# Performance work log

Measured on AMD Instinct MI355X. Metric: run time of the kernel, lower is better.

The kernel has to match this reference:

```python
import jax, jax.numpy as jnp
import numpy as np


def setup_inputs() -> dict:
    key = jax.random.key(0)
    k1, k2 = jax.random.split(key)
    B, M, N, D = 8, 2048, 2048, 1024
    x = jax.random.normal(k1, (B, M, D), dtype=jnp.float32)
    y = jax.random.normal(k2, (B, N, D), dtype=jnp.float32)
    return {"x": x, "y": y}


def reference(x, y):
    # scores e[b,m,n] = <x[b,m], y[b,n]>   (K.batch_dot(x, y, axes=2))
    e = jnp.einsum('bmd,bnd->bmn', x, y)
    # stable softmax over last axis (the exp/max/sum sequence in the original)
    p = jax.nn.softmax(e, axis=-1)
    # K.batch_dot(z, x, axes=1): contract axis 1 (m) of both -> [B, n, d]; V = x
    out = jnp.einsum('bmn,bmd->bnd', p, x)
    return out
```

## Files before the change

kernel.cpp:

```cpp
#include <hip/hip_runtime.h>
#include <hip/hip_bf16.h>
#include <stdint.h>

#define B_ 8
#define M_ 2048
#define N_ 2048
#define D_ 1024

typedef __bf16 bf16x8 __attribute__((ext_vector_type(8)));
typedef float f32x4 __attribute__((ext_vector_type(4)));
typedef uint16_t us4 __attribute__((ext_vector_type(4)));
typedef uint16_t us8 __attribute__((ext_vector_type(8)));

__device__ __forceinline__ uint16_t f2b(float f) {
    uint32_t u = __float_as_uint(f);
    return (uint16_t)((u + 0x7FFFu + ((u >> 16) & 1u)) >> 16);
}
__device__ __forceinline__ float b2f(uint16_t h) {
    return __uint_as_float(((uint32_t)h) << 16);
}

__device__ __forceinline__ void gld16(const uint16_t* g, const uint16_t* l) {
    __builtin_amdgcn_global_load_lds(
        (const __attribute__((address_space(1))) uint32_t*)g,
        (__attribute__((address_space(3))) uint32_t*)l,
        16, 0, 0);
}

__global__ __launch_bounds__(256) void k_split(const float* __restrict__ x,
                                               const float* __restrict__ y,
                                               uint16_t* __restrict__ xh, uint16_t* __restrict__ xl,
                                               uint16_t* __restrict__ yh, uint16_t* __restrict__ yl) {
    const int i = (blockIdx.x * 256 + threadIdx.x) * 4;
    float4 vx = *(const float4*)(x + i);
    float4 vy = *(const float4*)(y + i);
    float fx[4] = {vx.x, vx.y, vx.z, vx.w};
    float fy[4] = {vy.x, vy.y, vy.z, vy.w};
    us4 hx, lx, hy, ly;
#pragma unroll
    for (int k = 0; k < 4; ++k) {
        uint16_t h = f2b(fx[k]);
        hx[k] = h; lx[k] = f2b(fx[k] - b2f(h));
        uint16_t g = f2b(fy[k]);
        hy[k] = g; ly[k] = f2b(fy[k] - b2f(g));
    }
    *(us4*)(xh + i) = hx;
    *(us4*)(xl + i) = lx;
    *(us4*)(yh + i) = hy;
    *(us4*)(yl + i) = ly;
}

__global__ __launch_bounds__(512, 4) void k_gemm1(const uint16_t* __restrict__ xh,
                                                  const uint16_t* __restrict__ xl,
                                                  const uint16_t* __restrict__ yh,
                                                  const uint16_t* __restrict__ yl,
                                                  float* __restrict__ e,
                                                  float* __restrict__ pmax,
                                                  float* __restrict__ psum) {
    const int b = blockIdx.z;
    const int m0 = blockIdx.x * 128;
    const int n0 = blockIdx.y * 128;
    __shared__ __align__(16) uint16_t lds[32768];

    const int tid = threadIdx.x;
    const int lane = tid & 63;
    const int wid = tid >> 6;
    const int wm = (wid >> 2) * 64;
    const int wn = (wid & 3) * 32;
    const int quad = lane >> 4;
    const int r16 = lane & 15;
    const int swz8 = (quad ^ ((r16 >> 1) & 3)) * 8;

    const int row0 = wid * 16 + (lane >> 2);
    const int gd8 = ((lane & 3) ^ ((row0 >> 1) & 3)) * 8;
    const uint16_t* sp[4];
    sp[0] = xh + ((size_t)b * M_ + m0 + row0) * D_ + gd8;
    sp[1] = xl + ((size_t)b * M_ + m0 + row0) * D_ + gd8;
    sp[2] = yh + ((size_t)b * N_ + n0 + row0) * D_ + gd8;
    sp[3] = yl + ((size_t)b * N_ + n0 + row0) * D_ + gd8;
    const int ldsW = wid * 512;

    auto STAGE = [&](int dst, int ktn) {
#pragma unroll
        for (int c = 0; c < 4; ++c)
            gld16(sp[c] + ktn * 32, &lds[dst + c * 4096 + ldsW]);
    };

    const int abase = (wm + r16) * 32 + swz8;
    const int bbase = 8192 + (wn + r16) * 32 + swz8;

    f32x4 acc[4][2];
#pragma unroll
    for (int i = 0; i < 4; ++i)
#pragma unroll
        for (int j = 0; j < 2; ++j) acc[i][j] = (f32x4){0.f, 0.f, 0.f, 0.f};

    STAGE(0, 0);
    __syncthreads();

    for (int kt = 0; kt < D_ / 32; ++kt) {
        const int bo = (kt & 1) << 14;
        const int nbo = bo ^ 16384;
        if (kt < D_ / 32 - 1) STAGE(nbo, kt + 1);

        bf16x8 ah[4], al[4], bh[2], bl[2];
#pragma unroll
        for (int j = 0; j < 2; ++j) {
            bh[j] = *(const bf16x8*)&lds[bo + bbase + j * 512];
            bl[j] = *(const bf16x8*)&lds[bo + bbase + 4096 + j * 512];
        }
#pragma unroll
        for (int i = 0; i < 4; ++i) {
            ah[i] = *(const bf16x8*)&lds[bo + abase + i * 512];
            al[i] = *(const bf16x8*)&lds[bo + abase + 4096 + i * 512];
        }
#pragma unroll
        for (int i = 0; i < 4; ++i)
#pragma unroll
            for (int j = 0; j < 2; ++j) {
                acc[i][j] = __builtin_amdgcn_mfma_f32_16x16x32_bf16(ah[i], bh[j], acc[i][j], 0, 0, 0);
                acc[i][j] = __builtin_amdgcn_mfma_f32_16x16x32_bf16(ah[i], bl[j], acc[i][j], 0, 0, 0);
                acc[i][j] = __builtin_amdgcn_mfma_f32_16x16x32_bf16(al[i], bh[j], acc[i][j], 0, 0, 0);
            }
        __syncthreads();
    }

    float* eb = e + (size_t)b * M_ * N_;
    const int grows = (int)gridDim.z * M_;
    const int growbase = b * M_ + m0 + wm;
    const int nb = (n0 + wn) >> 5;
    float* pm = pmax + (size_t)nb * grows + growbase;
    float* ps = psum + (size_t)nb * grows + growbase;

#pragma unroll
    for (int i = 0; i < 4; ++i) {
#pragma unroll
        for (int r = 0; r < 4; ++r) {
            const float v0 = acc[i][0][r], v1 = acc[i][1][r];
            float mrow = fmaxf(v0, v1);
#pragma unroll
            for (int s = 1; s < 16; s <<= 1) mrow = fmaxf(mrow, __shfl_xor(mrow, s, 64));
            float srow_ = __expf(v0 - mrow) + __expf(v1 - mrow);
#pragma unroll
            for (int s = 1; s < 16; s <<= 1) srow_ += __shfl_xor(srow_, s, 64);
            const int lrow = i * 16 + quad * 4 + r;
            if (r16 == 0) { pm[lrow] = mrow; ps[lrow] = srow_; }
            const size_t ebase = (size_t)(m0 + wm + lrow) * N_ + n0 + wn + r16;
#pragma unroll
            for (int j = 0; j < 2; ++j) eb[ebase + j * 16] = acc[i][j][r];
        }
    }
}

__global__ __launch_bounds__(256) void k_combine(const float* __restrict__ pmax,
                                                 const float* __restrict__ psum,
                                                 float* __restrict__ mx,
                                                 float* __restrict__ inv, int rows) {
    const int r = blockIdx.x * 256 + threadIdx.x;
    float m = -3.4e38f;
#pragma unroll
    for (int nb = 0; nb < 64; ++nb) m = fmaxf(m, pmax[(size_t)nb * rows + r]);
    float s = 0.f;
#pragma unroll
    for (int nb = 0; nb < 64; ++nb)
        s += psum[(size_t)nb * rows + r] * __expf(pmax[(size_t)nb * rows + r] - m);
    mx[r] = m;
    inv[r] = 1.0f / s;
}

__global__ __launch_bounds__(256) void k_texp(const float* __restrict__ e,
                                              const float* __restrict__ mx,
                                              const float* __restrict__ inv,
                                              uint16_t* __restrict__ pT) {
    const int b = blockIdx.z, m0 = blockIdx.x * 64, n0 = blockIdx.y * 64;
    __shared__ float tile[64 * 65];
    const int t = threadIdx.x;
    const float* eb = e + (size_t)b * M_ * N_;
#pragma unroll
    for (int q = 0; q < 4; ++q) {
        const int row = q * 16 + (t >> 4);
        const int c4 = (t & 15) * 4;
        float4 v = *(const float4*)&eb[(size_t)(m0 + row) * N_ + n0 + c4];
        const float mv = mx[b * M_ + m0 + row];
        const float iv = inv[b * M_ + m0 + row];
        tile[row * 65 + c4 + 0] = __expf(v.x - mv) * iv;
        tile[row * 65 + c4 + 1] = __expf(v.y - mv) * iv;
        tile[row * 65 + c4 + 2] = __expf(v.z - mv) * iv;
        tile[row * 65 + c4 + 3] = __expf(v.w - mv) * iv;
    }
    __syncthreads();
    uint16_t* pb = pT + (size_t)b * N_ * M_;
#pragma unroll
    for (int q = 0; q < 2; ++q) {
        const int n = q * 32 + (t >> 3);
        const int mc = (t & 7) * 8;
        us8 o;
#pragma unroll
        for (int k = 0; k < 8; ++k) o[k] = f2b(tile[(mc + k) * 65 + n]);
        *(us8*)&pb[(size_t)(n0 + n) * M_ + m0 + mc] = o;
    }
}

__global__ __launch_bounds__(256) void k_tx(const float* __restrict__ x,
                                            uint16_t* __restrict__ xt) {
    const int b = blockIdx.z, m0 = blockIdx.x * 64, d0 = blockIdx.y * 64;
    __shared__ float tile[64 * 65];
    const int t = threadIdx.x;
    const float* xb = x + (size_t)b * M_ * D_;
#pragma unroll
    for (int q = 0; q < 4; ++q) {
        const int row = q * 16 + (t >> 4);
        const int c4 = (t & 15) * 4;
        float4 v = *(const float4*)&xb[(size_t)(m0 + row) * D_ + d0 + c4];
        tile[row * 65 + c4 + 0] = v.x;
        tile[row * 65 + c4 + 1] = v.y;
        tile[row * 65 + c4 + 2] = v.z;
        tile[row * 65 + c4 + 3] = v.w;
    }
    __syncthreads();
    uint16_t* xtb = xt + (size_t)b * D_ * M_;
#pragma unroll
    for (int q = 0; q < 2; ++q) {
        const int d = q * 32 + (t >> 3);
        const int mc = (t & 7) * 8;
        us8 o;
#pragma unroll
        for (int k = 0; k < 8; ++k) o[k] = f2b(tile[(mc + k) * 65 + d]);
        *(us8*)&xtb[(size_t)(d0 + d) * M_ + m0 + mc] = o;
    }
}

__global__ __launch_bounds__(256) void k_gemm2(const uint16_t* __restrict__ pT,
                                               const uint16_t* __restrict__ xt,
                                               float* __restrict__ out) {
    const int b = blockIdx.z;
    const int n0 = blockIdx.x * 128;
    const int d0 = blockIdx.y * 128;
    __shared__ __align__(16) uint16_t lds[32768];

    const int tid = threadIdx.x;
    const int lane = tid & 63;
    const int wid = tid >> 6;
    const int wn = (wid & 1) * 64;
    const int wd = (wid >> 1) * 64;
    const int quad = lane >> 4;
    const int r16 = lane & 15;

    const uint16_t* srcA = pT + ((size_t)b * N_ + n0) * M_;
    const uint16_t* srcB = xt + ((size_t)b * D_ + d0) * M_;

    f32x4 acc[4][4];
#pragma unroll
    for (int i = 0; i < 4; ++i)
#pragma unroll
        for (int j = 0; j < 4; ++j) acc[i][j] = (f32x4){0.f, 0.f, 0.f, 0.f};

    auto STAGE = [&](int dst, int kt) {
#pragma unroll
        for (int c = 0; c < 8; ++c) {
            const int offbase = c * 2048 + wid * 512;
            const int tile = offbase >> 13;
            const int o = (offbase & 8191) + lane * 8;
            const int row = o >> 6;
            const int gp = (o & 63) >> 3;
            const int gd = gp ^ (row & 7);
            const uint16_t* sp = tile ? srcB : srcA;
            gld16(sp + (size_t)row * M_ + kt * 64 + gd * 8, &lds[dst + offbase]);
        }
    };

    STAGE(0, 0);
    __syncthreads();

    for (int kt = 0; kt < M_ / 64; ++kt) {
        const int bo = (kt & 1) << 14;
        const int nbo = bo ^ 16384;
        if (kt < M_ / 64 - 1) STAGE(nbo, kt + 1);

#pragma unroll
        for (int h = 0; h < 2; ++h) {
            const int p = (h * 4 + quad) ^ (r16 & 7);
            bf16x8 a[4], bbr[4];
#pragma unroll
            for (int i = 0; i < 4; ++i) {
                a[i]   = *(const bf16x8*)&lds[bo + (wn + i * 16 + r16) * 64 + p * 8];
                bbr[i] = *(const bf16x8*)&lds[bo + 8192 + (wd + i * 16 + r16) * 64 + p * 8];
            }
#pragma unroll
            for (int i = 0; i < 4; ++i)
#pragma unroll
                for (int j = 0; j < 4; ++j)
                    acc[i][j] = __builtin_amdgcn_mfma_f32_16x16x32_bf16(a[i], bbr[j], acc[i][j], 0, 0, 0);
        }
        __syncthreads();
    }

    float* ob = out + (size_t)b * N_ * D_;
#pragma unroll
    for (int i = 0; i < 4; ++i) {
        const int rbase = n0 + wn + i * 16 + quad * 4;
#pragma unroll
        for (int j = 0; j < 4; ++j) {
            const int col = d0 + wd + j * 16 + r16;
#pragma unroll
            for (int r = 0; r < 4; ++r)
                ob[(size_t)(rbase + r) * D_ + col] = acc[i][j][r];
        }
    }
}

extern "C" void kernel_launch(void* const* d_in, const int* in_sizes, int n_in,
                              void* d_out, int out_size, void* d_ws, size_t ws_size,
                              hipStream_t stream) {
    const float* x = (const float*)d_in[0];
    const float* y = (const float*)d_in[1];
    float* out = (float*)d_out;
    char* ws = (char*)d_ws;

    const size_t MiB = 1024 * 1024;
    int g = 8;
    while (g > 1 && (size_t)g * 32 * MiB > ws_size) g >>= 1;
    if ((size_t)g * 32 * MiB > ws_size) return;

    const size_t T = (size_t)g * M_ * D_ * 2;
    uint16_t* xh = (uint16_t*)(ws + 0 * T);
    uint16_t* xl = (uint16_t*)(ws + 1 * T);
    uint16_t* yh = (uint16_t*)(ws + 2 * T);
    uint16_t* yl = (uint16_t*)(ws + 3 * T);
    float*    e  = (float*)(ws + 4 * T);
    float*    mx = (float*)(ws);
    float*    inv = mx + (size_t)g * M_;
    uint16_t* xt = xl;
    uint16_t* pT = yh;

    const size_t pelems = (size_t)64 * g * M_;
    float* pmax = (float*)d_out + (size_t)B_ * N_ * D_ - 2 * pelems;
    float* psum = pmax + pelems;

    for (int c0 = 0; c0 < B_; c0 += g) {
        const float* xc = x + (size_t)c0 * M_ * D_;
        const float* yc = y + (size_t)c0 * N_ * D_;
        float* oc = out + (size_t)c0 * N_ * D_;

        hipLaunchKernelGGL(k_split, dim3((g * M_ * D_) / (256 * 4)), dim3(256), 0, stream,
                           xc, yc, xh, xl, yh, yl);
        hipLaunchKernelGGL(k_gemm1, dim3(M_ / 128, N_ / 128, g), dim3(512), 0, stream,
                           xh, xl, yh, yl, e, pmax, psum);
        hipLaunchKernelGGL(k_combine, dim3((g * M_) / 256), dim3(256), 0, stream,
                           pmax, psum, mx, inv, g * M_);
        hipLaunchKernelGGL(k_texp, dim3(M_ / 64, N_ / 64, g), dim3(256), 0, stream,
                           e, mx, inv, pT);
        hipLaunchKernelGGL(k_tx, dim3(M_ / 64, D_ / 64, g), dim3(256), 0, stream, xc, xt);
        hipLaunchKernelGGL(k_gemm2, dim3(N_ / 128, D_ / 128, g), dim3(256), 0, stream,
                           pT, xt, oc);
    }
}
```

Measured before the change: 520.5 us.

## Enlarge gemm1 tile to 256x256 using 32x32x16 MFMA with s_setprio

The score GEMM's block tile grows from 128x128 to 256x256, and each wave now computes a 128x64 sub-tile with 32x32x16 bf16 MFMA instead of 16x16x32. LDS doubles to 128KB double-buffered, and each stage loads two 128-row halves per operand. The aim is more operand reuse per LDS read and fewer global loads per FLOP in the three-pass split-bf16 GEMM. The cost is lower occupancy (launch bound 2, fewer blocks: 256 instead of 1024), so there are fewer waves to hide latency and worse tail balance. The partial softmax max/sum blocks drop from 64 to 32 per row, and the combine kernel and workspace sizing change to match.

```diff
diff --git a/kernel.cpp b/kernel.cpp
--- a/kernel.cpp
+++ b/kernel.cpp
@@ -9,6 +9,7 @@
 
 typedef __bf16 bf16x8 __attribute__((ext_vector_type(8)));
 typedef float f32x4 __attribute__((ext_vector_type(4)));
+typedef float f32x16 __attribute__((ext_vector_type(16)));
 typedef uint16_t us4 __attribute__((ext_vector_type(4)));
 typedef uint16_t us8 __attribute__((ext_vector_type(8)));
 
@@ -50,7 +51,7 @@
     *(us4*)(yl + i) = ly;
 }
 
-__global__ __launch_bounds__(512, 4) void k_gemm1(const uint16_t* __restrict__ xh,
+__global__ __launch_bounds__(512, 2) void k_gemm1(const uint16_t* __restrict__ xh,
                                                   const uint16_t* __restrict__ xl,
                                                   const uint16_t* __restrict__ yh,
                                                   const uint16_t* __restrict__ yl,
@@ -58,96 +59,106 @@
                                                   float* __restrict__ pmax,
                                                   float* __restrict__ psum) {
     const int b = blockIdx.z;
-    const int m0 = blockIdx.x * 128;
-    const int n0 = blockIdx.y * 128;
-    __shared__ __align__(16) uint16_t lds[32768];
+    const int m0 = blockIdx.x * 256;
+    const int n0 = blockIdx.y * 256;
+    __shared__ __align__(16) uint16_t lds[65536];
 
     const int tid = threadIdx.x;
     const int lane = tid & 63;
     const int wid = tid >> 6;
-    const int wm = (wid >> 2) * 64;
-    const int wn = (wid & 3) * 32;
-    const int quad = lane >> 4;
-    const int r16 = lane & 15;
-    const int swz8 = (quad ^ ((r16 >> 1) & 3)) * 8;
-
-    const int row0 = wid * 16 + (lane >> 2);
-    const int gd8 = ((lane & 3) ^ ((row0 >> 1) & 3)) * 8;
-    const uint16_t* sp[4];
-    sp[0] = xh + ((size_t)b * M_ + m0 + row0) * D_ + gd8;
-    sp[1] = xl + ((size_t)b * M_ + m0 + row0) * D_ + gd8;
-    sp[2] = yh + ((size_t)b * N_ + n0 + row0) * D_ + gd8;
-    sp[3] = yl + ((size_t)b * N_ + n0 + row0) * D_ + gd8;
+    const int wm = (wid >> 2) * 128;
+    const int wn = (wid & 3) * 64;
+    const int l31 = lane & 31;
+    const int hi = lane >> 5;
+    const int swl = (l31 >> 1) & 3;
+
+    const int base_row = wid * 16 + (lane >> 2);
+    const int gd8 = ((lane & 3) ^ ((lane >> 3) & 3)) * 8;
+    const uint16_t* gp[4];
+    gp[0] = xh + ((size_t)b * M_ + m0 + base_row) * D_ + gd8;
+    gp[1] = xl + ((size_t)b * M_ + m0 + base_row) * D_ + gd8;
+    gp[2] = yh + ((size_t)b * N_ + n0 + base_row) * D_ + gd8;
+    gp[3] = yl + ((size_t)b * N_ + n0 + base_row) * D_ + gd8;
     const int ldsW = wid * 512;
 
     auto STAGE = [&](int dst, int ktn) {
 #pragma unroll
-        for (int c = 0; c < 4; ++c)
-            gld16(sp[c] + ktn * 32, &lds[dst + c * 4096 + ldsW]);
+        for (int c = 0; c < 8; ++c)
+            gld16(gp[c >> 1] + (size_t)(c & 1) * (128 * D_) + ktn * 32,
+                  &lds[dst + c * 4096 + ldsW]);
     };
 
-    const int abase = (wm + r16) * 32 + swz8;
-    const int bbase = 8192 + (wn + r16) * 32 + swz8;
-
-    f32x4 acc[4][2];
+    const int abase = (wm + l31) * 32;
+    const int bbase = 16384 + (wn + l31) * 32;
+
+    f32x16 acc[4][2];
 #pragma unroll
     for (int i = 0; i < 4; ++i)
 #pragma unroll
-        for (int j = 0; j < 2; ++j) acc[i][j] = (f32x4){0.f, 0.f, 0.f, 0.f};
+        for (int j = 0; j < 2; ++j)
+#pragma unroll
+            for (int r = 0; r < 16; ++r) acc[i][j][r] = 0.f;
 
     STAGE(0, 0);
     __syncthreads();
 
     for (int kt = 0; kt < D_ / 32; ++kt) {
-        const int bo = (kt & 1) << 14;
-        const int nbo = bo ^ 16384;
-        if (kt < D_ / 32 - 1) STAGE(nbo, kt + 1);
-
-        bf16x8 ah[4], al[4], bh[2], bl[2];
-#pragma unroll
-        for (int j = 0; j < 2; ++j) {
-            bh[j] = *(const bf16x8*)&lds[bo + bbase + j * 512];
-            bl[j] = *(const bf16x8*)&lds[bo + bbase + 4096 + j * 512];
-        }
-#pragma unroll
-        for (int i = 0; i < 4; ++i) {
-            ah[i] = *(const bf16x8*)&lds[bo + abase + i * 512];
-            al[i] = *(const bf16x8*)&lds[bo + abase + 4096 + i * 512];
-        }
-#pragma unroll
-        for (int i = 0; i < 4; ++i)
+        const int bo = (kt & 1) << 15;
+        if (kt < D_ / 32 - 1) STAGE(bo ^ 32768, kt + 1);
+
+#pragma unroll
+        for (int kc = 0; kc < 2; ++kc) {
+            const int g8 = ((hi + 2 * kc) ^ swl) * 8;
+            bf16x8 ah[4], al[4], bh[2], bl[2];
 #pragma unroll
             for (int j = 0; j < 2; ++j) {
-                acc[i][j] = __builtin_amdgcn_mfma_f32_16x16x32_bf16(ah[i], bh[j], acc[i][j], 0, 0, 0);
-                acc[i][j] = __builtin_amdgcn_mfma_f32_16x16x32_bf16(ah[i], bl[j], acc[i][j], 0, 0, 0);
-                acc[i][j] = __builtin_amdgcn_mfma_f32_16x16x32_bf16(al[i], bh[j], acc[i][j], 0, 0, 0);
+                const int o = bo + bbase + j * 1024 + g8;
+                bh[j] = *(const bf16x8*)&lds[o];
+                bl[j] = *(const bf16x8*)&lds[o + 8192];
             }
+#pragma unroll
+            for (int i = 0; i < 4; ++i) {
+                const int o = bo + abase + i * 1024 + g8;
+                ah[i] = *(const bf16x8*)&lds[o];
+                al[i] = *(const bf16x8*)&lds[o + 8192];
+            }
+            __builtin_amdgcn_s_setprio(1);
+#pragma unroll
+            for (int i = 0; i < 4; ++i)
+#pragma unroll
+                for (int j = 0; j < 2; ++j) {
+                    acc[i][j] = __builtin_amdgcn_mfma_f32_32x32x16_bf16(ah[i], bh[j], acc[i][j], 0, 0, 0);
+                    acc[i][j] = __builtin_amdgcn_mfma_f32_32x32x16_bf16(ah[i], bl[j], acc[i][j], 0, 0, 0);
+                    acc[i][j] = __builtin_amdgcn_mfma_f32_32x32x16_bf16(al[i], bh[j], acc[i][j], 0, 0, 0);
+                }
+            __builtin_amdgcn_s_setprio(0);
+        }
         __syncthreads();
     }
 
     float* eb = e + (size_t)b * M_ * N_;
     const int grows = (int)gridDim.z * M_;
     const int growbase = b * M_ + m0 + wm;
-    const int nb = (n0 + wn) >> 5;
+    const int nb = (n0 + wn) >> 6;
     float* pm = pmax + (size_t)nb * grows + growbase;
     float* ps = psum + (size_t)nb * grows + growbase;
 
 #pragma unroll
     for (int i = 0; i < 4; ++i) {
 #pragma unroll
-        for (int r = 0; r < 4; ++r) {
-            const float v0 = acc[i][0][r], v1 = acc[i][1][r];
+        for (int reg = 0; reg < 16; ++reg) {
+            const float v0 = acc[i][0][reg], v1 = acc[i][1][reg];
             float mrow = fmaxf(v0, v1);
 #pragma unroll
-            for (int s = 1; s < 16; s <<= 1) mrow = fmaxf(mrow, __shfl_xor(mrow, s, 64));
+            for (int s = 1; s < 32; s <<= 1) mrow = fmaxf(mrow, __shfl_xor(mrow, s, 64));
             float srow_ = __expf(v0 - mrow) + __expf(v1 - mrow);
 #pragma unroll
-            for (int s = 1; s < 16; s <<= 1) srow_ += __shfl_xor(srow_, s, 64);
-            const int lrow = i * 16 + quad * 4 + r;
-            if (r16 == 0) { pm[lrow] = mrow; ps[lrow] = srow_; }
-            const size_t ebase = (size_t)(m0 + wm + lrow) * N_ + n0 + wn + r16;
-#pragma unroll
-            for (int j = 0; j < 2; ++j) eb[ebase + j * 16] = acc[i][j][r];
+            for (int s = 1; s < 32; s <<= 1) srow_ += __shfl_xor(srow_, s, 64);
+            const int lrow = i * 32 + (reg & 3) + 8 * (reg >> 2) + 4 * hi;
+            if (l31 == 0) { pm[lrow] = mrow; ps[lrow] = srow_; }
+            const size_t ebase = (size_t)(m0 + wm + lrow) * N_ + n0 + wn + l31;
+            eb[ebase] = v0;
+            eb[ebase + 32] = v1;
         }
     }
 }
@@ -159,10 +170,10 @@
     const int r = blockIdx.x * 256 + threadIdx.x;
     float m = -3.4e38f;
 #pragma unroll
-    for (int nb = 0; nb < 64; ++nb) m = fmaxf(m, pmax[(size_t)nb * rows + r]);
+    for (int nb = 0; nb < 32; ++nb) m = fmaxf(m, pmax[(size_t)nb * rows + r]);
     float s = 0.f;
 #pragma unroll
-    for (int nb = 0; nb < 64; ++nb)
+    for (int nb = 0; nb < 32; ++nb)
         s += psum[(size_t)nb * rows + r] * __expf(pmax[(size_t)nb * rows + r] - m);
     mx[r] = m;
     inv[r] = 1.0f / s;
@@ -333,7 +344,7 @@
     uint16_t* xt = xl;
     uint16_t* pT = yh;
 
-    const size_t pelems = (size_t)64 * g * M_;
+    const size_t pelems = (size_t)32 * g * M_;
     float* pmax = (float*)d_out + (size_t)B_ * N_ * D_ - 2 * pelems;
     float* psum = pmax + pelems;
 
@@ -344,7 +355,7 @@
 
         hipLaunchKernelGGL(k_split, dim3((g * M_ * D_) / (256 * 4)), dim3(256), 0, stream,
                            xc, yc, xh, xl, yh, yl);
-        hipLaunchKernelGGL(k_gemm1, dim3(M_ / 128, N_ / 128, g), dim3(512), 0, stream,
+        hipLaunchKernelGGL(k_gemm1, dim3(M_ / 256, N_ / 256, g), dim3(512), 0, stream,
                            xh, xl, yh, yl, e, pmax, psum);
         hipLaunchKernelGGL(k_combine, dim3((g * M_) / 256), dim3(256), 0, stream,
                            pmax, psum, mx, inv, g * M_);
```

Result: no change. 524.2 us (+0.7%).
